# Kernel optimization log

Measured on AMD Instinct MI355X. Metric: run time of the kernel, lower is better.

Reference implementation:

```python
import jax, jax.numpy as jnp
import numpy as np

# Model dims
D = 2048        # hidden_size
H = 16          # num_heads
KVH = 8         # num_key_value_heads
DH = 128        # head_dim
NUM_SLOTS = 16  # state-cache slots
B = 4           # prefill segments (regularized ragged batch)
L = 2048        # tokens per segment
T = B * L
C = 64          # GLA chunk size (fused_chunk_gla)
NEG = -1e30


def setup_inputs() -> dict:
    key = jax.random.key(0)
    k0, k1, k2, k3 = jax.random.split(key, 4)
    hidden_states = jax.random.normal(k0, (T, D), jnp.float32)
    W_qkv = jax.random.normal(k1, (D, (H + 2 * KVH) * DH), jnp.float32) * 0.02
    b_qkv = jnp.zeros(((H + 2 * KVH) * DH,), jnp.float32)
    kv_cache = jax.random.normal(k2, (NUM_SLOTS, H, DH, DH), jnp.float32) * 0.1
    state_indices = jax.random.randint(k3, (B,), 0, NUM_SLOTS, jnp.int32)
    return {"hidden_states": hidden_states, "W_qkv": W_qkv, "b_qkv": b_qkv,
            "kv_cache": kv_cache, "state_indices": state_indices}


def _to_chunks(x):
    # [T, H, d] -> [n_chunks, B, C, H, d]
    return x.reshape(B, L // C, C, H, DH).transpose(1, 0, 2, 3, 4)


def _gla_chunk_body(mask):
    def body(S, inp):
        # S: [B,H,dk,dv]; qc/kc/vc/gc: [B,C,H,d]
        qc, kc, vc, gc = inp
        Bc = jnp.cumsum(gc, axis=1)                       # inclusive log-decay within chunk
        # inter-chunk: initial state decayed by exp(Bc)
        o_inter = jnp.einsum('bchk,bhkv->bchv', qc * jnp.exp(Bc), S)
        # intra-chunk causal scores: A_ij = sum_d q_i,d * exp(B_i - B_j)_d * k_j,d, j<=i
        diff = Bc[:, :, None] - Bc[:, None, :]            # [B,Ci,Cj,H,dk], <=0 on lower tri
        diff = jnp.where(mask[None, :, :, None, None], diff, NEG)
        A = jnp.einsum('bihk,bijhk,bjhk->bijh', qc, jnp.exp(diff), kc)
        o = o_inter + jnp.einsum('bijh,bjhv->bihv', A, vc)
        # state update: S' = diag(exp(B_last)) S + sum_j (k_j exp(B_last - B_j)) v_j^T
        b_last = Bc[:, -1]                                # [B,H,dk]
        kg = kc * jnp.exp(b_last[:, None] - Bc)
        S_new = S * jnp.exp(b_last)[..., None] + jnp.einsum('bchk,bchv->bhkv', kg, vc)
        return S_new, o
    return jax.checkpoint(body)


def _forward(hidden_states, W_qkv, b_qkv, kv_cache, state_indices):
    qkv = hidden_states @ W_qkv + b_qkv
    q = qkv[:, :H * DH].reshape(T, H, DH)
    k = qkv[:, H * DH:(H + KVH) * DH].reshape(T, KVH, DH)
    v = qkv[:, (H + KVH) * DH:].reshape(T, KVH, DH)
    n_rep = H // KVH
    k = jnp.repeat(k, n_rep, axis=1)                      # repeat_kv (3D branch)
    v = jnp.repeat(v, n_rep, axis=1)
    q = jax.nn.relu(q) * DH ** -0.5                       # q_feature_map + fused_chunk_gla scale
    k = jnp.minimum(jax.nn.sigmoid(k), 0.95)              # sigmoid + clamp(max=clamp_max)
    g = jnp.log1p(-k)                                     # (1 - k).log()

    S0 = kv_cache[state_indices]                          # [B,H,dk,dv] per-slot initial states
    mask = jnp.tril(jnp.ones((C, C), bool))
    _, o = jax.lax.scan(_gla_chunk_body(mask), S0,
                        (_to_chunks(q), _to_chunks(k), _to_chunks(v), _to_chunks(g)))
    # [n_chunks,B,C,H,dv] -> per-segment concat [T, H*dv]
    return o.transpose(1, 0, 2, 3, 4).reshape(T, H * DH)


def reference(hidden_states, W_qkv, b_qkv, kv_cache, state_indices):
    return _forward(hidden_states, W_qkv, b_qkv, kv_cache, state_indices)
```

## Files before the change

kernel.cpp:

```cpp
#include <hip/hip_runtime.h>
#include <hip/hip_bf16.h>
#include <math.h>

#define RSQRT_DH 0.08838834764831845f

typedef __attribute__((ext_vector_type(8))) short short8;
typedef __attribute__((ext_vector_type(4))) float floatx4;

#define BAR() do { asm volatile("" ::: "memory"); __builtin_amdgcn_s_barrier(); asm volatile("" ::: "memory"); } while (0)

static __device__ __forceinline__ float bf2f(unsigned short u) {
  return __uint_as_float(((unsigned int)u) << 16);
}
static __device__ __forceinline__ unsigned short f2bf(float f) {
  unsigned int x = __float_as_uint(f);
  return (unsigned short)((x + 0x7fffu + ((x >> 16) & 1u)) >> 16);
}
static __device__ __forceinline__ ushort4 f4bf(float a, float b, float c, float d) {
  ushort4 r; r.x = f2bf(a); r.y = f2bf(b); r.z = f2bf(c); r.w = f2bf(d); return r;
}
static __device__ __forceinline__ short8 ld8u(const unsigned short* p) {
  short4 a = *(const short4*)p;
  short4 b = *(const short4*)(p + 4);
  short8 r;
  r[0] = a.x; r[1] = a.y; r[2] = a.z; r[3] = a.w;
  r[4] = b.x; r[5] = b.y; r[6] = b.z; r[7] = b.w;
  return r;
}

__launch_bounds__(256)
__global__ void k_cvt(const float* __restrict__ in, unsigned short* __restrict__ out, int n4) {
  int i = blockIdx.x * 256 + threadIdx.x;
  if (i >= n4) return;
  float4 v = ((const float4*)in)[i];
  ((ushort4*)out)[i] = f4bf(v.x, v.y, v.z, v.w);
}

__launch_bounds__(256)
__global__ void k_cvt_wt(const float* __restrict__ W, unsigned short* __restrict__ Wt) {
  __shared__ float tile[32][33];
  int t = threadIdx.x;
  int c = t & 31, r = t >> 5;
  int bx = blockIdx.x, by = blockIdx.y;
#pragma unroll
  for (int j = 0; j < 4; ++j)
    tile[r + j * 8][c] = W[(size_t)(by * 32 + r + j * 8) * 4096 + bx * 32 + c];
  __syncthreads();
#pragma unroll
  for (int j = 0; j < 4; ++j)
    Wt[(size_t)(bx * 32 + r + j * 8) * 2048 + by * 32 + c] = f2bf(tile[c][r + j * 8]);
}

__launch_bounds__(512, 2)
__global__ void k_gemm(const unsigned short* __restrict__ A,
                       const unsigned short* __restrict__ Bt,
                       const float* __restrict__ bias,
                       unsigned short* __restrict__ qb,
                       unsigned short* __restrict__ kb,
                       unsigned short* __restrict__ vb,
                       float* __restrict__ gf) {
  __shared__ unsigned short lds[65536];

  const int tid = threadIdx.x;
  const int w = tid >> 6, l = tid & 63;
  const int wm = w >> 2, wn = w & 3;
  const int lr = l & 15, quad = l >> 4;

  const int id = blockIdx.x;
  const int swz = (id & 7) * 64 + (id >> 3);
  const int bm = swz >> 4, bn = swz & 15;
  const int m0 = bm * 256, n0 = bn * 256;

  const int srow = tid >> 2;
  const int scol = (((tid & 3) ^ ((tid >> 3) & 3)) << 3);
  const unsigned short* agp = A + (size_t)(m0 + srow) * 2048 + scol;
  const unsigned short* bgp = Bt + (size_t)(n0 + srow) * 2048 + scol;
  unsigned short* ldsA_dst = lds + w * 512;
  unsigned short* ldsB_dst = lds + 8192 + w * 512;

  auto stageA = [&](int d, int u, int ktile) {
    __builtin_amdgcn_global_load_lds(
        (const __attribute__((address_space(1))) void*)(agp + (size_t)u * 262144 + (size_t)ktile * 32),
        (__attribute__((address_space(3))) void*)(ldsA_dst + d * 16384 + u * 4096),
        16, 0, 0);
  };
  auto stageB = [&](int d, int u, int ktile) {
    __builtin_amdgcn_global_load_lds(
        (const __attribute__((address_space(1))) void*)(bgp + (size_t)u * 262144 + (size_t)ktile * 32),
        (__attribute__((address_space(3))) void*)(ldsB_dst + d * 16384 + u * 4096),
        16, 0, 0);
  };

  const int kcol = ((quad ^ ((lr >> 1) & 3)) << 3);
  const int arow_base = (wm * 128 + lr) * 32 + kcol;
  const int brow_base = (wn * 64 + lr) * 32 + kcol;

  floatx4 acc[8][4] = {};

#pragma unroll
  for (int pt = 0; pt < 3; ++pt) {
    stageA(pt, 0, pt); stageA(pt, 1, pt);
    stageB(pt, 0, pt); stageB(pt, 1, pt);
  }

  for (int t = 0; t < 64; ++t) {
    const int d = t & 3;
    const unsigned short* Ab = lds + d * 16384;
    const unsigned short* Bb = Ab + 8192;
    const int t3 = t + 3;
    const int d3 = t3 & 3;

    if (t < 62)       asm volatile("s_waitcnt vmcnt(8)" ::: "memory");
    else if (t == 62) asm volatile("s_waitcnt vmcnt(4)" ::: "memory");
    else              asm volatile("s_waitcnt vmcnt(0)" ::: "memory");
    BAR();

    short8 af[4], bfr[4];
#pragma unroll
    for (int i = 0; i < 4; ++i) af[i] = *(const short8*)(Ab + arow_base + i * 512);
#pragma unroll
    for (int i = 0; i < 4; ++i) bfr[i] = *(const short8*)(Bb + brow_base + i * 512);
    if (t3 < 64) { stageA(d3, 0, t3); stageA(d3, 1, t3); }
    __builtin_amdgcn_s_setprio(1);
#pragma unroll
    for (int mi = 0; mi < 4; ++mi)
#pragma unroll
      for (int ni = 0; ni < 4; ++ni)
        acc[mi][ni] = __builtin_amdgcn_mfma_f32_16x16x32_bf16(af[mi], bfr[ni], acc[mi][ni], 0, 0, 0);
    __builtin_amdgcn_s_setprio(0);

    BAR();

#pragma unroll
    for (int i = 0; i < 4; ++i) af[i] = *(const short8*)(Ab + arow_base + 2048 + i * 512);
    if (t3 < 64) { stageB(d3, 0, t3); stageB(d3, 1, t3); }
    __builtin_amdgcn_s_setprio(1);
#pragma unroll
    for (int mi = 0; mi < 4; ++mi)
#pragma unroll
      for (int ni = 0; ni < 4; ++ni)
        acc[4 + mi][ni] = __builtin_amdgcn_mfma_f32_16x16x32_bf16(af[mi], bfr[ni], acc[4 + mi][ni], 0, 0, 0);
    __builtin_amdgcn_s_setprio(0);
  }

  const int lm0 = m0 + wm * 128 + quad * 4;
  const int ln0 = n0 + wn * 64 + lr;
#pragma unroll
  for (int ni = 0; ni < 4; ++ni) {
    const int col = ln0 + ni * 16;
    const float bnv = bias[col];
#pragma unroll
    for (int mi = 0; mi < 8; ++mi) {
#pragma unroll
      for (int r = 0; r < 4; ++r) {
        const int row = lm0 + mi * 16 + r;
        float val = acc[mi][ni][r] + bnv;
        if (col < 2048) {
          qb[(size_t)row * 2048 + col] = f2bf(fmaxf(val, 0.f) * RSQRT_DH);
        } else if (col < 3072) {
          float s = 1.f / (1.f + __expf(-val));
          s = fminf(s, 0.95f);
          size_t idx = (size_t)row * 1024 + (col - 2048);
          kb[idx] = f2bf(s);
          gf[idx] = log1pf(-s);
        } else {
          vb[(size_t)row * 1024 + (col - 3072)] = f2bf(val);
        }
      }
    }
  }
}

__launch_bounds__(256)
__global__ void k_phaseA(const unsigned short* __restrict__ kb,
                         const unsigned short* __restrict__ vb,
                         const float* __restrict__ gf,
                         float* __restrict__ blast,
                         unsigned short* __restrict__ Pb) {
  __shared__ float sBc[64 * 128];
  __shared__ float sKg[64 * 128];
  const int t = threadIdx.x;
  const int chunk = blockIdx.x, chain = blockIdx.y;
  const int b = chain >> 4, h = chain & 15, kvh = h >> 1;
  const int t0 = b * 2048 + chunk * 64;

#pragma unroll
  for (int rep = 0; rep < 8; ++rep) {
    int e = rep * 256 + t;
    int i = e >> 5, d4 = e & 31;
    *(float4*)(sBc + i * 128 + d4 * 4) =
        *(const float4*)(gf + (size_t)(t0 + i) * 1024 + kvh * 128 + d4 * 4);
  }
  __syncthreads();
  if (t < 128) {
    float run = sBc[t];
    for (int i = 1; i < 64; ++i) { run += sBc[i * 128 + t]; sBc[i * 128 + t] = run; }
    blast[((size_t)chain * 32 + chunk) * 128 + t] = run;
  }
  __syncthreads();
#pragma unroll
  for (int rep = 0; rep < 32; ++rep) {
    int e = rep * 256 + t;
    int i = e >> 7, d = e & 127;
    float kk = bf2f(kb[(size_t)(t0 + i) * 1024 + kvh * 128 + d]);
    sKg[e] = kk * __expf(sBc[63 * 128 + d] - sBc[e]);
  }
  __syncthreads();
  const int kq = t >> 3, vq = t & 7;
  const int kd0 = kq * 4, vd0 = vq * 16;
  float acc[4][16] = {};
  const unsigned short* vrow = vb + (size_t)t0 * 1024 + kvh * 128 + vd0;
  for (int i = 0; i < 64; ++i) {
    float4 kg4 = *(const float4*)(sKg + i * 128 + kd0);
    float ka[4] = {kg4.x, kg4.y, kg4.z, kg4.w};
    ushort4 v0 = *(const ushort4*)(vrow + (size_t)i * 1024);
    ushort4 v1 = *(const ushort4*)(vrow + (size_t)i * 1024 + 4);
    ushort4 v2 = *(const ushort4*)(vrow + (size_t)i * 1024 + 8);
    ushort4 v3 = *(const ushort4*)(vrow + (size_t)i * 1024 + 12);
    float vf[16] = {bf2f(v0.x), bf2f(v0.y), bf2f(v0.z), bf2f(v0.w),
                    bf2f(v1.x), bf2f(v1.y), bf2f(v1.z), bf2f(v1.w),
                    bf2f(v2.x), bf2f(v2.y), bf2f(v2.z), bf2f(v2.w),
                    bf2f(v3.x), bf2f(v3.y), bf2f(v3.z), bf2f(v3.w)};
#pragma unroll
    for (int r = 0; r < 4; ++r)
#pragma unroll
      for (int j = 0; j < 16; ++j) acc[r][j] += ka[r] * vf[j];
  }
  size_t pbase = ((size_t)chain * 32 + chunk) * 16384;
#pragma unroll
  for (int r = 0; r < 4; ++r)
#pragma unroll
    for (int j4 = 0; j4 < 4; ++j4)
      *(ushort4*)(Pb + pbase + (size_t)(kd0 + r) * 128 + vd0 + j4 * 4) =
          f4bf(acc[r][j4 * 4], acc[r][j4 * 4 + 1], acc[r][j4 * 4 + 2], acc[r][j4 * 4 + 3]);
}

__launch_bounds__(256)
__global__ void k_scan(const float* __restrict__ kv_cache,
                       const int* __restrict__ sidx,
                       const float* __restrict__ blast,
                       const unsigned short* __restrict__ Pb,
                       unsigned short* __restrict__ Sb) {
  const int t = threadIdx.x;
  const int part = blockIdx.x;
  const int chain = blockIdx.y;
  const int b = chain >> 4, h = chain & 15;
  const int e0 = part * 1024 + t * 4;
  const int kd = e0 >> 7;
  const int slot = sidx[b];
  float4 s = *(const float4*)(kv_cache + ((size_t)slot * 16 + h) * 16384 + e0);
#pragma unroll 1
  for (int c = 0; c < 32; ++c) {
    *(ushort4*)(Sb + ((size_t)c * 64 + chain) * 16384 + e0) = f4bf(s.x, s.y, s.z, s.w);
    float eb = __expf(blast[((size_t)chain * 32 + c) * 128 + kd]);
    ushort4 p = *(const ushort4*)(Pb + ((size_t)chain * 32 + c) * 16384 + e0);
    s.x = s.x * eb + bf2f(p.x);
    s.y = s.y * eb + bf2f(p.y);
    s.z = s.z * eb + bf2f(p.z);
    s.w = s.w * eb + bf2f(p.w);
  }
}

__launch_bounds__(256)
__global__ void k_output(const unsigned short* __restrict__ qb,
                         const unsigned short* __restrict__ kb,
                         const unsigned short* __restrict__ vb,
                         const float* __restrict__ gf,
                         const unsigned short* __restrict__ Sb,
                         float* __restrict__ out) {
  __shared__ float sBc[64 * 128];
  __shared__ unsigned short sR3[11136];
  unsigned short* sA   = sR3;
  unsigned short* sKE  = sR3 + 4608;
  unsigned short* sQE2 = sR3 + 4608 + 4352;
  unsigned short* sQE0 = sR3;
  unsigned short* sSt  = sR3 + 4608;
  unsigned short* sVt  = sR3 + 4608;

  const int t = threadIdx.x;
  const int w = t >> 6, l = t & 63;
  const int lr = l & 15, quad = l >> 4;
  const int chunk = blockIdx.x, chain = blockIdx.y;
  const int b = chain >> 4, h = chain & 15, kvh = h >> 1;
  const int t0 = b * 2048 + chunk * 64;
  const size_t sbase = ((size_t)chunk * 64 + chain) * 16384;

#pragma unroll
  for (int rep = 0; rep < 8; ++rep) {
    int e = rep * 256 + t, i = e >> 5, d4 = e & 31;
    *(float4*)(sBc + i * 128 + d4 * 4) =
        *(const float4*)(gf + (size_t)(t0 + i) * 1024 + kvh * 128 + d4 * 4);
  }
  __syncthreads();
  if (t < 128) {
    float run = sBc[t];
#pragma unroll
    for (int i = 1; i < 64; ++i) { run += sBc[i * 128 + t]; sBc[i * 128 + t] = run; }
  }

  floatx4 o[8];
#pragma unroll
  for (int i = 0; i < 8; ++i) o[i] = 0.f;

#pragma unroll
  for (int kh = 0; kh < 2; ++kh) {
    __syncthreads();
#pragma unroll
    for (int rep = 0; rep < 2; ++rep) {
      int idx = rep * 256 + t;
      int i = idx >> 3, g = idx & 7;
      int k0 = kh * 64 + g * 8;
      short8 q8 = *(const short8*)(qb + (size_t)(t0 + i) * 2048 + h * 128 + k0);
      short8 r;
#pragma unroll
      for (int u = 0; u < 8; ++u)
        r[u] = (short)f2bf(bf2f((unsigned short)q8[u]) * __expf(sBc[i * 128 + k0 + u]));
      *(short8*)(sQE0 + i * 72 + g * 8) = r;
    }
#pragma unroll
    for (int vh = 0; vh < 2; ++vh) {
      __syncthreads();
#pragma unroll
      for (int rep = 0; rep < 2; ++rep) {
        int idx = rep * 256 + t;
        int kl = idx >> 3, g = idx & 7;
        short8 s8 = *(const short8*)(Sb + sbase + (size_t)(kh * 64 + kl) * 128 + vh * 64 + g * 8);
#pragma unroll
        for (int u = 0; u < 8; ++u) sSt[(g * 8 + u) * 76 + kl] = (unsigned short)s8[u];
      }
      __syncthreads();
      short8 af0 = *(const short8*)(sQE0 + (w * 16 + lr) * 72 + quad * 8);
      short8 af1 = *(const short8*)(sQE0 + (w * 16 + lr) * 72 + 32 + quad * 8);
#pragma unroll
      for (int tv = 0; tv < 4; ++tv) {
        const unsigned short* bp = sSt + (tv * 16 + lr) * 76 + quad * 8;
        short8 bf0 = ld8u(bp);
        short8 bf1 = ld8u(bp + 32);
        o[vh * 4 + tv] = __builtin_amdgcn_mfma_f32_16x16x32_bf16(af0, bf0, o[vh * 4 + tv], 0, 0, 0);
        o[vh * 4 + tv] = __builtin_amdgcn_mfma_f32_16x16x32_bf16(af1, bf1, o[vh * 4 + tv], 0, 0, 0);
      }
    }
  }

  __syncthreads();
  for (int idx = t; idx < 576; idx += 256)
    *(short8*)(sA + idx * 8) = (short8)0;
#pragma unroll
  for (int I = 0; I < 4; ++I) {
    const float* Rrow = (I > 0) ? (sBc + (I * 16 - 1) * 128) : nullptr;
    for (int base = 0; base < (I + 1) * 16; base += 32) {
      int nrows = min(32, (I + 1) * 16 - base);
      __syncthreads();
      int ngroups = nrows * 16;
      for (int idx = t; idx < ngroups; idx += 256) {
        int jl = idx >> 4, g = idx & 15;
        int j = base + jl, k0 = g * 8;
        short8 k8 = *(const short8*)(kb + (size_t)(t0 + j) * 1024 + kvh * 128 + k0);
        short8 r;
#pragma unroll
        for (int u = 0; u < 8; ++u) {
          int k = k0 + u;
          float Rk = Rrow ? Rrow[k] : 0.f;
          r[u] = (short)f2bf(bf2f((unsigned short)k8[u]) * __expf(Rk - sBc[j * 128 + k]));
        }
        *(short8*)(sKE + jl * 136 + k0) = r;
      }
      if (base == 0) {
        {
          int idx = t;
          int il = idx >> 4, g = idx & 15;
          int i = I * 16 + il, k0 = g * 8;
          short8 q8 = *(const short8*)(qb + (size_t)(t0 + i) * 2048 + h * 128 + k0);
          short8 r;
#pragma unroll
          for (int u = 0; u < 8; ++u) {
            int k = k0 + u;
            float Rk = Rrow ? Rrow[k] : 0.f;
            r[u] = (short)f2bf(bf2f((unsigned short)q8[u]) * __expf(sBc[i * 128 + k] - Rk));
          }
          *(short8*)(sQE2 + il * 136 + k0) = r;
        }
      }
      __syncthreads();
      const int J = w;
      if (J * 16 >= base && J * 16 < base + nrows) {
        floatx4 a4 = {};
#pragma unroll
        for (int ks = 0; ks < 4; ++ks) {
          short8 afr = *(const short8*)(sQE2 + lr * 136 + ks * 32 + quad * 8);
          short8 bfr = *(const short8*)(sKE + (J * 16 - base + lr) * 136 + ks * 32 + quad * 8);
          a4 = __builtin_amdgcn_mfma_f32_16x16x32_bf16(afr, bfr, a4, 0, 0, 0);
        }
#pragma unroll
        for (int r = 0; r < 4; ++r) {
          int il = quad * 4 + r;
          float v = ((J < I) || (lr <= il)) ? a4[r] : 0.f;
          sA[(I * 16 + il) * 72 + J * 16 + lr] = f2bf(v);
        }
      }
    }
  }

  __syncthreads();
  short8 aA0 = *(const short8*)(sA + (w * 16 + lr) * 72 + quad * 8);
  short8 aA1 = *(const short8*)(sA + (w * 16 + lr) * 72 + 32 + quad * 8);
#pragma unroll
  for (int vh = 0; vh < 2; ++vh) {
    if (vh) __syncthreads();
#pragma unroll
    for (int rep = 0; rep < 2; ++rep) {
      int idx = rep * 256 + t;
      int j = idx >> 3, g = idx & 7;
      short8 v8 = *(const short8*)(vb + (size_t)(t0 + j) * 1024 + kvh * 128 + vh * 64 + g * 8);
#pragma unroll
      for (int u = 0; u < 8; ++u) sVt[(g * 8 + u) * 76 + j] = (unsigned short)v8[u];
    }
    __syncthreads();
#pragma unroll
    for (int tv = 0; tv < 4; ++tv) {
      const unsigned short* bp = sVt + (tv * 16 + lr) * 76 + quad * 8;
      short8 b0 = ld8u(bp);
      short8 b1 = ld8u(bp + 32);
      o[vh * 4 + tv] = __builtin_amdgcn_mfma_f32_16x16x32_bf16(aA0, b0, o[vh * 4 + tv], 0, 0, 0);
      o[vh * 4 + tv] = __builtin_amdgcn_mfma_f32_16x16x32_bf16(aA1, b1, o[vh * 4 + tv], 0, 0, 0);
    }
  }

#pragma unroll
  for (int tv8 = 0; tv8 < 8; ++tv8) {
    int col = (tv8 >> 2) * 64 + (tv8 & 3) * 16 + lr;
#pragma unroll
    for (int r = 0; r < 4; ++r) {
      int i = w * 16 + quad * 4 + r;
      out[(size_t)(t0 + i) * 2048 + h * 128 + col] = o[tv8][r];
    }
  }
}

extern "C" void kernel_launch(void* const* d_in, const int* in_sizes, int n_in,
                              void* d_out, int out_size, void* d_ws, size_t ws_size,
                              hipStream_t stream) {
  (void)in_sizes; (void)n_in; (void)out_size; (void)ws_size;
  const float* hs   = (const float*)d_in[0];
  const float* W    = (const float*)d_in[1];
  const float* bias = (const float*)d_in[2];
  const float* kvc  = (const float*)d_in[3];
  const int*   sidx = (const int*)d_in[4];

  char* ws = (char*)d_ws;
  unsigned short* Sb  = (unsigned short*)(ws + 0);
  unsigned short* hsb = (unsigned short*)(ws + 0);
  unsigned short* wtb = (unsigned short*)(ws + 33554432);
  unsigned short* qb  = (unsigned short*)(ws + 67108864);
  unsigned short* kb  = (unsigned short*)(ws + 100663296);
  unsigned short* vb  = (unsigned short*)(ws + 117440512);
  float*          gf  = (float*)(ws + 134217728);
  float*          bl  = (float*)(ws + 167772160);
  unsigned short* Pb  = (unsigned short*)d_out;
  float* out = (float*)d_out;

  k_cvt<<<dim3(16384), dim3(256), 0, stream>>>(hs, hsb, 16777216 / 4);
  k_cvt_wt<<<dim3(128, 64), dim3(256), 0, stream>>>(W, wtb);
  k_gemm<<<dim3(512), dim3(512), 0, stream>>>(hsb, wtb, bias, qb, kb, vb, gf);
  k_phaseA<<<dim3(32, 64), dim3(256), 0, stream>>>(kb, vb, gf, bl, Pb);
  k_scan<<<dim3(16, 64), dim3(256), 0, stream>>>(kvc, sidx, bl, Pb, Sb);
  k_output<<<dim3(32, 64), dim3(256), 0, stream>>>(qb, kb, vb, gf, Sb, out);
}
```

Baseline: 698.1 us.

## Stage GEMM epilogue through LDS for vectorized coalesced stores and remap tile swizzle

The GEMM epilogue now writes accumulators into shared memory in 32-row slabs, then each thread reads four contiguous columns and issues vectorized 8-byte bf16 and 16-byte float stores per row. This replaces scattered 2-byte and 4-byte per-element stores, and the per-element column branch becomes a per-block branch on n0. The block-to-tile mapping also changes from a strided swizzle to 8x8 tile groups per XCD, aiming for better L2 reuse of the A and B tiles. In exchange the epilogue adds eight extra barrier rounds and an LDS round trip.

```diff
diff --git a/kernel.cpp b/kernel.cpp
--- a/kernel.cpp
+++ b/kernel.cpp
@@ -67,8 +67,9 @@
   const int lr = l & 15, quad = l >> 4;
 
   const int id = blockIdx.x;
-  const int swz = (id & 7) * 64 + (id >> 3);
-  const int bm = swz >> 4, bn = swz & 15;
+  const int x = id & 7, loc = id >> 3;
+  const int bm = (x >> 1) * 8 + (loc >> 3);
+  const int bn = (x & 1) * 8 + (loc & 7);
   const int m0 = bm * 256, n0 = bn * 256;
 
   const int srow = tid >> 2;
@@ -143,31 +144,51 @@
     __builtin_amdgcn_s_setprio(0);
   }
 
-  const int lm0 = m0 + wm * 128 + quad * 4;
-  const int ln0 = n0 + wn * 64 + lr;
-#pragma unroll
-  for (int ni = 0; ni < 4; ++ni) {
-    const int col = ln0 + ni * 16;
-    const float bnv = bias[col];
-#pragma unroll
-    for (int mi = 0; mi < 8; ++mi) {
-#pragma unroll
-      for (int r = 0; r < 4; ++r) {
-        const int row = lm0 + mi * 16 + r;
-        float val = acc[mi][ni][r] + bnv;
-        if (col < 2048) {
-          qb[(size_t)row * 2048 + col] = f2bf(fmaxf(val, 0.f) * RSQRT_DH);
-        } else if (col < 3072) {
-          float s = 1.f / (1.f + __expf(-val));
-          s = fminf(s, 0.95f);
-          size_t idx = (size_t)row * 1024 + (col - 2048);
-          kb[idx] = f2bf(s);
-          gf[idx] = log1pf(-s);
-        } else {
-          vb[(size_t)row * 1024 + (col - 3072)] = f2bf(val);
-        }
-      }
-    }
+  float* ldsf = (float*)lds;
+  __syncthreads();
+
+  float4 bv;
+  {
+    const float* bp = bias + n0 + l * 4;
+    bv.x = bp[0]; bv.y = bp[1]; bv.z = bp[2]; bv.w = bp[3];
+  }
+
+#pragma unroll
+  for (int a = 0; a < 8; ++a) {
+#pragma unroll
+    for (int ni = 0; ni < 4; ++ni)
+#pragma unroll
+      for (int r = 0; r < 4; ++r)
+        ldsf[(wm * 16 + quad * 4 + r) * 268 + wn * 64 + ni * 16 + lr] = acc[a][ni][r];
+    __syncthreads();
+
+    const int rbase = m0 + (a >> 2) * 64 + (a & 3) * 16;
+#pragma unroll
+    for (int it = 0; it < 4; ++it) {
+      const int row32 = w * 4 + it;
+      const int grow = rbase + (row32 >> 4) * 128 + (row32 & 15);
+      float4 f = *(const float4*)&ldsf[row32 * 268 + l * 4];
+      f.x += bv.x; f.y += bv.y; f.z += bv.z; f.w += bv.w;
+      if (n0 < 2048) {
+        *(ushort4*)(qb + (size_t)grow * 2048 + n0 + l * 4) =
+            f4bf(fmaxf(f.x, 0.f) * RSQRT_DH, fmaxf(f.y, 0.f) * RSQRT_DH,
+                 fmaxf(f.z, 0.f) * RSQRT_DH, fmaxf(f.w, 0.f) * RSQRT_DH);
+      } else if (n0 < 3072) {
+        float sx = fminf(1.f / (1.f + __expf(-f.x)), 0.95f);
+        float sy = fminf(1.f / (1.f + __expf(-f.y)), 0.95f);
+        float sz = fminf(1.f / (1.f + __expf(-f.z)), 0.95f);
+        float sw = fminf(1.f / (1.f + __expf(-f.w)), 0.95f);
+        size_t idx = (size_t)grow * 1024 + (n0 - 2048) + l * 4;
+        *(ushort4*)(kb + idx) = f4bf(sx, sy, sz, sw);
+        float4 g4; g4.x = log1pf(-sx); g4.y = log1pf(-sy);
+        g4.z = log1pf(-sz); g4.w = log1pf(-sw);
+        *(float4*)(gf + idx) = g4;
+      } else {
+        *(ushort4*)(vb + (size_t)grow * 1024 + (n0 - 3072) + l * 4) =
+            f4bf(f.x, f.y, f.z, f.w);
+      }
+    }
+    if (a < 7) __syncthreads();
   }
 }
 
```

Measured after the change: 588.9 us. -15.6%, faster.
